# Kernel tuning notes

Measured on AMD Instinct MI355X. Metric: run time of the kernel, lower is better.

## Reference

```python
import jax, jax.numpy as jnp
import numpy as np

B, N, C, H = 16, 1024, 768, 12
D = C // H
SCALE = D ** -0.5


def setup_inputs() -> dict:
    key = jax.random.key(0)
    k1, k2, k3, k4, k5 = jax.random.split(key, 5)
    return {
        "x": jax.random.normal(k1, (B, N, C), dtype=jnp.float32),
        "qkv_w": jax.random.normal(k2, (3 * C, C), dtype=jnp.float32) * (C ** -0.5),
        "qkv_b": jax.random.normal(k3, (3 * C,), dtype=jnp.float32) * 0.02,
        "proj_w": jax.random.normal(k4, (C, C), dtype=jnp.float32) * (C ** -0.5),
        "proj_b": jax.random.normal(k5, (C,), dtype=jnp.float32) * 0.02,
    }


def reference(x, qkv_w, qkv_b, proj_w, proj_b):
    # x: [B, N, C]. torch Linear: y = x @ W.T + b
    b, n, c = x.shape
    qkv = x @ qkv_w.T + qkv_b                      # [B, N, 3C]
    qkv = qkv.reshape(b, n, 3, H, D).transpose(2, 0, 3, 1, 4)  # [3, B, H, N, D]
    q, k, v = qkv[0], qkv[1], qkv[2]
    # dropout is identity in eval mode; scores scaled by head_dim**-0.5
    scores = jnp.einsum("bhnd,bhmd->bhnm", q, k) * SCALE  # [B, H, N, N]
    attn = jax.nn.softmax(scores, axis=-1)
    out = jnp.einsum("bhnm,bhmd->bhnd", attn, v)           # [B, H, N, D]
    out = out.transpose(0, 2, 1, 3).reshape(b, n, c)       # [B, N, C]
    return out @ proj_w.T + proj_b
```

## Files before the change

### kernel.cpp

```cpp
#include <hip/hip_runtime.h>
#include <hip/hip_bf16.h>


typedef __attribute__((ext_vector_type(8))) short short8;
typedef __attribute__((ext_vector_type(4))) float floatx4;
typedef __attribute__((ext_vector_type(16))) float floatx16;
typedef __attribute__((ext_vector_type(2))) unsigned int uint2v;

constexpr int Bsz = 16, Nseq = 1024, Cdim = 768, Hh = 12, Dd = 64;
constexpr float QSC = 0.1803368801f;
constexpr int LDV = Bsz * Nseq;

__device__ __forceinline__ ushort f2bs(float f) {
    union { __hip_bfloat16 h; ushort u; } cv;
    cv.h = __float2bfloat16(f);
    return cv.u;
}
__device__ __forceinline__ void stF(float* p, float v) { *p = v; }
__device__ __forceinline__ void stF(ushort* p, float v) { *p = f2bs(v); }

__device__ __forceinline__ float fexp2(float x) {
#if __has_builtin(__builtin_amdgcn_exp2f)
    return __builtin_amdgcn_exp2f(x);
#else
    return exp2f(x);
#endif
}

__device__ __forceinline__ void gld16(void* lds, const void* g) {
    __builtin_amdgcn_global_load_lds(
        (const __attribute__((address_space(1))) unsigned int*)g,
        (__attribute__((address_space(3))) unsigned int*)lds, 16, 0, 0);
}

__global__ __launch_bounds__(256) void pack_bf16(
        const float* __restrict__ x, const float* __restrict__ w1,
        const float* __restrict__ w2, ushort* __restrict__ xb,
        ushort* __restrict__ w1b, ushort* __restrict__ w2b) {
    const size_t n0 = (size_t)Bsz * Nseq * Cdim;
    const size_t n1 = (size_t)3 * Cdim * Cdim;
    size_t i = ((size_t)blockIdx.x * 256 + threadIdx.x) * 4;
    const float* src;
    ushort* dst;
    if (i < n0) { src = x; dst = xb; }
    else if (i < n0 + n1) { i -= n0; src = w1; dst = w1b; }
    else { i -= n0 + n1; src = w2; dst = w2b; }
    float4 v = *(const float4*)&src[i];
    *(ushort4*)&dst[i] = make_ushort4(f2bs(v.x), f2bs(v.y), f2bs(v.z), f2bs(v.w));
}

template <typename TO>
__global__ __launch_bounds__(256) void gemm_nt_mfma(
        const ushort* __restrict__ A, const ushort* __restrict__ Bw,
        const float* __restrict__ bias, TO* __restrict__ C0,
        int ld0, int M, int N, int K, int bias_row, int qsplit, float qscale) {
    __shared__ ushort As[128 * 64];
    __shared__ ushort Bs[128 * 64];
    const int t = threadIdx.x;
    const int lane = t & 63;
    const int w = t >> 6;
    const int quad = lane >> 4;
    const int l16 = lane & 15;
    const int m0 = blockIdx.y * 128;
    const int n0 = blockIdx.x * 128;
    const int mw = (w >> 1) * 64;
    const int nw = (w & 1) * 64;
    const int srow = lane >> 3;
    const int schunk = lane & 7;

    floatx4 acc[4][4];
#pragma unroll
    for (int i = 0; i < 4; ++i)
#pragma unroll
        for (int j = 0; j < 4; ++j) acc[i][j] = (floatx4)0.0f;

    for (int k0 = 0; k0 < K; k0 += 64) {
        __syncthreads();
#pragma unroll
        for (int i = 0; i < 4; ++i) {
            int r0 = (w * 4 + i) * 8;
            int row = r0 + srow;
            int cs = (schunk ^ (row & 7)) * 8;
            gld16(&As[r0 * 64], &A[(size_t)(m0 + row) * K + k0 + cs]);
            gld16(&Bs[r0 * 64], &Bw[(size_t)(n0 + row) * K + k0 + cs]);
        }
        __syncthreads();

#pragma unroll
        for (int kk = 0; kk < 2; ++kk) {
            const int pc = ((kk * 4 + quad) ^ (l16 & 7)) * 8;
            short8 af[4], bfr[4];
#pragma unroll
            for (int i = 0; i < 4; ++i)
                af[i] = *(const short8*)&As[(mw + i * 16 + l16) * 64 + pc];
#pragma unroll
            for (int j = 0; j < 4; ++j)
                bfr[j] = *(const short8*)&Bs[(nw + j * 16 + l16) * 64 + pc];
#pragma unroll
            for (int i = 0; i < 4; ++i)
#pragma unroll
                for (int j = 0; j < 4; ++j)
                    acc[i][j] = __builtin_amdgcn_mfma_f32_16x16x32_bf16(
                        af[i], bfr[j], acc[i][j], 0, 0, 0);
        }
    }

    if (bias_row) {
        float brv[4][4];
#pragma unroll
        for (int i = 0; i < 4; ++i)
#pragma unroll
            for (int r = 0; r < 4; ++r)
                brv[i][r] = bias[m0 + mw + i * 16 + quad * 4 + r];
#pragma unroll
        for (int j = 0; j < 4; ++j) {
            int col = n0 + nw + j * 16 + l16;
#pragma unroll
            for (int i = 0; i < 4; ++i)
#pragma unroll
                for (int r = 0; r < 4; ++r) {
                    int row = m0 + mw + i * 16 + quad * 4 + r;
                    stF(&C0[(size_t)row * ld0 + col], acc[i][j][r] + brv[i][r]);
                }
        }
    } else {
#pragma unroll
        for (int j = 0; j < 4; ++j) {
            int col = n0 + nw + j * 16 + l16;
            float bc = bias[col];
            float sc = (col < qsplit) ? qscale : 1.0f;
#pragma unroll
            for (int i = 0; i < 4; ++i)
#pragma unroll
                for (int r = 0; r < 4; ++r) {
                    int row = m0 + mw + i * 16 + quad * 4 + r;
                    stF(&C0[(size_t)row * ld0 + col], (acc[i][j][r] + bc) * sc);
                }
        }
    }
}

__global__ __launch_bounds__(256, 3) void attn_mfma(
        const ushort* __restrict__ qk, const ushort* __restrict__ vt,
        ushort* __restrict__ outp) {
    __shared__ ushort Ks[2][64 * 64];
    __shared__ ushort Vts[2][64 * 64];

    const int t = threadIdx.x;
    const int lane = t & 63;
    const int w = t >> 6;
    const int l32 = lane & 31;
    const int hi = lane >> 5;
    const int srow = lane >> 3;
    const int schunk = lane & 7;

    const int bid = blockIdx.x;
    const int qt = (bid >> 3) & 7;
    const int bh = (bid & 7) + 8 * (bid >> 6);
    const int h = bh % Hh, b = bh / Hh;

    const size_t rs = 2 * Cdim;
    const ushort* qbase = qk + (size_t)b * Nseq * rs + h * Dd;
    const ushort* kbase = qbase + Cdim;
    const ushort* vbase = vt + (size_t)(h * Dd) * LDV + (size_t)b * Nseq;

    short8 aq[4];
    {
        int q = qt * 128 + w * 32 + l32;
#pragma unroll
        for (int kc = 0; kc < 4; ++kc)
            aq[kc] = *(const short8*)&qbase[(size_t)q * rs + kc * 16 + hi * 8];
    }

    auto stage = [&](int kt64, int buf) {
#pragma unroll
        for (int i = 0; i < 2; ++i) {
            int r0 = (w * 2 + i) * 8;
            int row = r0 + srow;
            int cs = (schunk ^ (row & 7)) * 8;
            gld16(&Ks[buf][r0 * 64], &kbase[(size_t)(kt64 * 64 + row) * rs + cs]);
            gld16(&Vts[buf][r0 * 64], &vbase[(size_t)row * LDV + kt64 * 64 + cs]);
        }
    };

    floatx16 o[2];
    o[0] = (floatx16)0.0f;
    o[1] = (floatx16)0.0f;
    float lsum = 0.f;

    stage(0, 0);
    for (int kt = 0; kt < Nseq / 64; ++kt) {
        __syncthreads();
        if (kt + 1 < Nseq / 64) stage(kt + 1, (kt + 1) & 1);
        const ushort* Kb = Ks[kt & 1];
        const ushort* Vb = Vts[kt & 1];

        floatx16 st[2];
        st[0] = (floatx16)0.0f;
        st[1] = (floatx16)0.0f;
#pragma unroll
        for (int kc = 0; kc < 4; ++kc) {
            const int cs = ((kc * 2 + hi) ^ (l32 & 7)) * 8;
            short8 ak0 = *(const short8*)&Kb[l32 * 64 + cs];
            short8 ak1 = *(const short8*)&Kb[(32 + l32) * 64 + cs];
            st[0] = __builtin_amdgcn_mfma_f32_32x32x16_bf16(ak0, aq[kc], st[0], 0, 0, 0);
            st[1] = __builtin_amdgcn_mfma_f32_32x32x16_bf16(ak1, aq[kc], st[1], 0, 0, 0);
        }

#pragma unroll
        for (int km = 0; km < 2; ++km) {
            float p[16];
#pragma unroll
            for (int r = 0; r < 16; ++r) p[r] = fexp2(st[km][r]);
            lsum += (((p[0] + p[1]) + (p[2] + p[3])) +
                     ((p[4] + p[5]) + (p[6] + p[7]))) +
                    (((p[8] + p[9]) + (p[10] + p[11])) +
                     ((p[12] + p[13]) + (p[14] + p[15])));
            uint c[8];
#pragma unroll
            for (int i = 0; i < 8; ++i) {
                union { __hip_bfloat162 h2; uint u; } cv;
                cv.h2 = __float22bfloat162_rn(make_float2(p[2 * i], p[2 * i + 1]));
                c[i] = cv.u;
            }
            uint wd[8];
#if __has_builtin(__builtin_amdgcn_permlane32_swap)
            uint2v r02 = __builtin_amdgcn_permlane32_swap(c[0], c[2], false, false);
            uint2v r13 = __builtin_amdgcn_permlane32_swap(c[1], c[3], false, false);
            uint2v r46 = __builtin_amdgcn_permlane32_swap(c[4], c[6], false, false);
            uint2v r57 = __builtin_amdgcn_permlane32_swap(c[5], c[7], false, false);
            wd[0] = r02.x; wd[2] = r02.y;
            wd[1] = r13.x; wd[3] = r13.y;
            wd[4] = r46.x; wd[6] = r46.y;
            wd[5] = r57.x; wd[7] = r57.y;
#else
            uint x0 = __shfl_xor(c[0], 32), x1 = __shfl_xor(c[1], 32);
            uint x2 = __shfl_xor(c[2], 32), x3 = __shfl_xor(c[3], 32);
            uint x4 = __shfl_xor(c[4], 32), x5 = __shfl_xor(c[5], 32);
            uint x6 = __shfl_xor(c[6], 32), x7 = __shfl_xor(c[7], 32);
            wd[0] = hi ? x2 : c[0]; wd[1] = hi ? x3 : c[1];
            wd[2] = hi ? c[2] : x0; wd[3] = hi ? c[3] : x1;
            wd[4] = hi ? x6 : c[4]; wd[5] = hi ? x7 : c[5];
            wd[6] = hi ? c[6] : x4; wd[7] = hi ? c[7] : x5;
#endif
            union { uint u[4]; short8 s; } af0, af1;
            af0.u[0] = wd[0]; af0.u[1] = wd[1]; af0.u[2] = wd[2]; af0.u[3] = wd[3];
            af1.u[0] = wd[4]; af1.u[1] = wd[5]; af1.u[2] = wd[6]; af1.u[3] = wd[7];

#pragma unroll
            for (int dblk = 0; dblk < 2; ++dblk) {
                const int row = dblk * 32 + l32;
#pragma unroll
                for (int ks = 0; ks < 2; ++ks) {
                    const int ch = ((km * 4 + ks * 2 + hi) ^ (l32 & 7)) * 8;
                    short8 bv = *(const short8*)&Vb[row * 64 + ch];
                    o[dblk] = __builtin_amdgcn_mfma_f32_32x32x16_bf16(
                        ks ? af1.s : af0.s, bv, o[dblk], 0, 0, 0);
                }
            }
        }
    }

    float lf = lsum + __shfl_xor(lsum, 32);
    float linv = __builtin_amdgcn_rcpf(lf);

    const int qg0 = qt * 128 + w * 32;
#pragma unroll
    for (int r = 0; r < 16; ++r) {
        int rowq = (r & 3) + 8 * (r >> 2) + 4 * hi;
        float li = __shfl(linv, rowq);
        int q = qg0 + rowq;
#pragma unroll
        for (int dblk = 0; dblk < 2; ++dblk) {
            int d = dblk * 32 + l32;
            outp[((size_t)(b * Nseq + q)) * Cdim + h * Dd + d] =
                f2bs(o[dblk][r] * li);
        }
    }
}

extern "C" void kernel_launch(void* const* d_in, const int* in_sizes, int n_in,
                              void* d_out, int out_size, void* d_ws, size_t ws_size,
                              hipStream_t stream) {
    const float* x      = (const float*)d_in[0];
    const float* qkv_w  = (const float*)d_in[1];
    const float* qkv_b  = (const float*)d_in[2];
    const float* proj_w = (const float*)d_in[3];
    const float* proj_b = (const float*)d_in[4];
    float* out = (float*)d_out;

    const int M = Bsz * Nseq;
    ushort* xb    = (ushort*)d_ws;
    ushort* qk    = xb + (size_t)M * Cdim;
    ushort* vtbuf = qk + (size_t)M * 2 * Cdim;
    ushort* wqkvb = vtbuf + (size_t)Cdim * M;
    ushort* wprjb = wqkvb + (size_t)3 * Cdim * Cdim;
    ushort* attnout = xb;

    pack_bf16<<<14592, 256, 0, stream>>>(x, qkv_w, proj_w, xb, wqkvb, wprjb);
    gemm_nt_mfma<ushort><<<dim3(12, 128), 256, 0, stream>>>(
        xb, wqkvb, qkv_b, qk, 2 * Cdim, M, 2 * Cdim, Cdim, 0, Cdim, QSC);
    gemm_nt_mfma<ushort><<<dim3(128, 6), 256, 0, stream>>>(
        wqkvb + (size_t)2 * Cdim * Cdim, xb, qkv_b + 2 * Cdim, vtbuf,
        M, Cdim, M, Cdim, 1, 0, 1.0f);
    attn_mfma<<<Bsz * Hh * (Nseq / 128), 256, 0, stream>>>(qk, vtbuf, attnout);
    gemm_nt_mfma<float><<<dim3(6, 128), 256, 0, stream>>>(
        attnout, wprjb, proj_b, out, Cdim, M, Cdim, Cdim, 0, 0, 1.0f);
}
```

Before: 299.3 us.

## Double-buffer GEMM LDS tiles, remap blocks across XCDs, raise MFMA priority

The GEMM now splits K into 32-wide steps and double-buffers the A/B tiles in shared memory. The next tile is issued before the current one is computed, and one barrier per step replaces two. Block indices are remapped so consecutive tiles group onto the same XCD, which is meant to improve L2 reuse. s_setprio is also wrapped around the MFMA sections in both the GEMM and the attention kernel. In exchange there are more loop iterations with smaller MFMA batches, and the block remap assumes the grid size is a multiple of 8.

```diff
diff --git a/kernel.cpp b/kernel.cpp
--- a/kernel.cpp
+++ b/kernel.cpp
@@ -54,19 +54,25 @@
         const ushort* __restrict__ A, const ushort* __restrict__ Bw,
         const float* __restrict__ bias, TO* __restrict__ C0,
         int ld0, int M, int N, int K, int bias_row, int qsplit, float qscale) {
-    __shared__ ushort As[128 * 64];
-    __shared__ ushort Bs[128 * 64];
+    __shared__ ushort As[2][128 * 32];
+    __shared__ ushort Bs[2][128 * 32];
     const int t = threadIdx.x;
     const int lane = t & 63;
     const int w = t >> 6;
     const int quad = lane >> 4;
     const int l16 = lane & 15;
-    const int m0 = blockIdx.y * 128;
-    const int n0 = blockIdx.x * 128;
+
+    const int nwg = gridDim.x * gridDim.y;
+    const int bidl = blockIdx.y * gridDim.x + blockIdx.x;
+    const int cpx = nwg >> 3;
+    const int s = (bidl & 7) * cpx + (bidl >> 3);
+    const int m0 = (s / gridDim.x) * 128;
+    const int n0 = (s % gridDim.x) * 128;
+
     const int mw = (w >> 1) * 64;
     const int nw = (w & 1) * 64;
-    const int srow = lane >> 3;
-    const int schunk = lane & 7;
+    const int srow = lane >> 2;
+    const int schunk = lane & 3;
 
     floatx4 acc[4][4];
 #pragma unroll
@@ -74,35 +80,41 @@
 #pragma unroll
         for (int j = 0; j < 4; ++j) acc[i][j] = (floatx4)0.0f;
 
-    for (int k0 = 0; k0 < K; k0 += 64) {
+    auto stage = [&](int k0, int buf) {
+#pragma unroll
+        for (int i = 0; i < 2; ++i) {
+            int r0 = (w * 2 + i) * 16;
+            int row = r0 + srow;
+            int cs = (schunk ^ (row & 3)) * 8;
+            gld16(&As[buf][r0 * 32], &A[(size_t)(m0 + row) * K + k0 + cs]);
+            gld16(&Bs[buf][r0 * 32], &Bw[(size_t)(n0 + row) * K + k0 + cs]);
+        }
+    };
+
+    const int nk = K / 32;
+    stage(0, 0);
+    for (int ki = 0; ki < nk; ++ki) {
         __syncthreads();
-#pragma unroll
-        for (int i = 0; i < 4; ++i) {
-            int r0 = (w * 4 + i) * 8;
-            int row = r0 + srow;
-            int cs = (schunk ^ (row & 7)) * 8;
-            gld16(&As[r0 * 64], &A[(size_t)(m0 + row) * K + k0 + cs]);
-            gld16(&Bs[r0 * 64], &Bw[(size_t)(n0 + row) * K + k0 + cs]);
-        }
-        __syncthreads();
-
-#pragma unroll
-        for (int kk = 0; kk < 2; ++kk) {
-            const int pc = ((kk * 4 + quad) ^ (l16 & 7)) * 8;
-            short8 af[4], bfr[4];
-#pragma unroll
-            for (int i = 0; i < 4; ++i)
-                af[i] = *(const short8*)&As[(mw + i * 16 + l16) * 64 + pc];
+        if (ki + 1 < nk) stage((ki + 1) * 32, (ki + 1) & 1);
+        const ushort* Ab = As[ki & 1];
+        const ushort* Bb = Bs[ki & 1];
+
+        const int pc = (quad ^ (l16 & 3)) * 8;
+        short8 af[4], bfr[4];
+#pragma unroll
+        for (int i = 0; i < 4; ++i)
+            af[i] = *(const short8*)&Ab[(mw + i * 16 + l16) * 32 + pc];
+#pragma unroll
+        for (int j = 0; j < 4; ++j)
+            bfr[j] = *(const short8*)&Bb[(nw + j * 16 + l16) * 32 + pc];
+        __builtin_amdgcn_s_setprio(1);
+#pragma unroll
+        for (int i = 0; i < 4; ++i)
 #pragma unroll
             for (int j = 0; j < 4; ++j)
-                bfr[j] = *(const short8*)&Bs[(nw + j * 16 + l16) * 64 + pc];
-#pragma unroll
-            for (int i = 0; i < 4; ++i)
-#pragma unroll
-                for (int j = 0; j < 4; ++j)
-                    acc[i][j] = __builtin_amdgcn_mfma_f32_16x16x32_bf16(
-                        af[i], bfr[j], acc[i][j], 0, 0, 0);
-        }
+                acc[i][j] = __builtin_amdgcn_mfma_f32_16x16x32_bf16(
+                    af[i], bfr[j], acc[i][j], 0, 0, 0);
+        __builtin_amdgcn_s_setprio(0);
     }
 
     if (bias_row) {
@@ -198,6 +210,7 @@
         floatx16 st[2];
         st[0] = (floatx16)0.0f;
         st[1] = (floatx16)0.0f;
+        __builtin_amdgcn_s_setprio(1);
 #pragma unroll
         for (int kc = 0; kc < 4; ++kc) {
             const int cs = ((kc * 2 + hi) ^ (l32 & 7)) * 8;
@@ -206,6 +219,7 @@
             st[0] = __builtin_amdgcn_mfma_f32_32x32x16_bf16(ak0, aq[kc], st[0], 0, 0, 0);
             st[1] = __builtin_amdgcn_mfma_f32_32x32x16_bf16(ak1, aq[kc], st[1], 0, 0, 0);
         }
+        __builtin_amdgcn_s_setprio(0);
 
 #pragma unroll
         for (int km = 0; km < 2; ++km) {
@@ -247,6 +261,7 @@
             af0.u[0] = wd[0]; af0.u[1] = wd[1]; af0.u[2] = wd[2]; af0.u[3] = wd[3];
             af1.u[0] = wd[4]; af1.u[1] = wd[5]; af1.u[2] = wd[6]; af1.u[3] = wd[7];
 
+            __builtin_amdgcn_s_setprio(1);
 #pragma unroll
             for (int dblk = 0; dblk < 2; ++dblk) {
                 const int row = dblk * 32 + l32;
@@ -258,6 +273,7 @@
                         ks ? af1.s : af0.s, bv, o[dblk], 0, 0, 0);
                 }
             }
+            __builtin_amdgcn_s_setprio(0);
         }
     }
 
```

After: 317.3 us. 6.0% more time.
